# Performance work log

Measured on AMD Instinct MI355X. Metric: run time of the kernel, lower is better.

## Reference

```python
import jax, jax.numpy as jnp
import numpy as np

HIDDEN = 1024
FFN = 4096
NUM_EXPERTS = 8
LB_WEIGHT = 0.01
BATCH, SEQ = 4, 1024


def setup_inputs() -> dict:
    key = jax.random.key(0)
    ks = jax.random.split(key, 6)
    s_h = 1.0 / np.sqrt(HIDDEN)
    s_f = 1.0 / np.sqrt(FFN)
    return {
        "x": jax.random.normal(ks[0], (BATCH, SEQ, HIDDEN), dtype=jnp.float32),
        "router_w": jax.random.uniform(ks[1], (NUM_EXPERTS, HIDDEN), jnp.float32, -s_h, s_h),
        "fc1_w": jax.random.uniform(ks[2], (NUM_EXPERTS, FFN, HIDDEN), jnp.float32, -s_h, s_h),
        "fc1_b": jax.random.uniform(ks[3], (NUM_EXPERTS, FFN), jnp.float32, -s_h, s_h),
        "fc2_w": jax.random.uniform(ks[4], (NUM_EXPERTS, HIDDEN, FFN), jnp.float32, -s_f, s_f),
        "fc2_b": jax.random.uniform(ks[5], (NUM_EXPERTS, HIDDEN), jnp.float32, -s_f, s_f),
    }


def reference(x, router_w, fc1_w, fc1_b, fc2_w, fc2_b):
    B, S, H = x.shape
    E = router_w.shape[0]
    T = B * S
    xf = x.reshape(T, H)

    # Router: top-1 over softmax probs
    logits = xf @ router_w.T                     # [T, E]
    probs = jax.nn.softmax(logits, axis=-1)      # [T, E]
    expert_weights = jnp.max(probs, axis=-1)     # [T]
    expert_idx = jnp.argmax(probs, axis=-1)      # [T] int

    # Expert MLPs computed densely for all experts (faithful math; jit-friendly
    # replacement for the dynamic-shaped per-expert gather/scatter).
    h = jax.nn.gelu(jnp.einsum('td,efd->etf', xf, fc1_w) + fc1_b[:, None, :],
                    approximate=False)                      # [E, T, F]
    out_all = jnp.einsum('etf,ehf->eth', h, fc2_w) + fc2_b[:, None, :]  # [E, T, H]

    # Select each token's assigned expert output, scaled by its gate weight.
    out_flat = out_all[expert_idx, jnp.arange(T)] * expert_weights[:, None]  # [T, H]
    output = out_flat.reshape(B, S, H)

    # Load balance loss
    mean_probs = probs.mean(axis=0)                                   # [E]
    counts = jnp.bincount(expert_idx, length=E).astype(jnp.float32)   # [E]
    freq = counts / T
    aux_loss = LB_WEIGHT * E * jnp.sum(mean_probs * freq)
    return output, aux_loss
```

## Files before the change

### kernel.cpp

```cpp
#include <hip/hip_runtime.h>
#include <cstdint>

#define HID 1024
#define FFN 4096
#define NE 8
#define NT 4096

typedef __bf16 bf16x8 __attribute__((ext_vector_type(8)));
typedef unsigned short ushortx8 __attribute__((ext_vector_type(8)));
typedef float f32x4 __attribute__((ext_vector_type(4)));


__device__ __forceinline__ unsigned pk_bf16(float a, float b) {
  unsigned ua = __float_as_uint(a), ub = __float_as_uint(b);
  ua = (ua + 0x7fffu + ((ua >> 16) & 1u)) >> 16;
  ub = (ub + 0x7fffu + ((ub >> 16) & 1u)) >> 16;
  return ua | (ub << 16);
}
__device__ __forceinline__ unsigned short f2bf(float a) {
  unsigned ua = __float_as_uint(a);
  return (unsigned short)((ua + 0x7fffu + ((ua >> 16) & 1u)) >> 16);
}

__global__ __launch_bounds__(256) void router_kernel(
    const float* __restrict__ x, const float* __restrict__ rw,
    int* __restrict__ counts, float* __restrict__ prob_sum,
    int* __restrict__ eidx, float* __restrict__ wgt) {
  __shared__ float rsm[NE * HID];
  __shared__ float pshare[4][NE];
  for (int i = threadIdx.x; i < NE * HID; i += 256) rsm[i] = rw[i];
  __syncthreads();
  int wave = threadIdx.x >> 6, lane = threadIdx.x & 63;
  int t = blockIdx.x * 4 + wave;
  const float* xr = x + (size_t)t * HID;
  float acc[NE];
#pragma unroll
  for (int e = 0; e < NE; e++) acc[e] = 0.f;
#pragma unroll
  for (int j = 0; j < HID / 64; j++) {
    float xv = xr[j * 64 + lane];
#pragma unroll
    for (int e = 0; e < NE; e++) acc[e] = fmaf(xv, rsm[e * HID + j * 64 + lane], acc[e]);
  }
#pragma unroll
  for (int off = 32; off > 0; off >>= 1) {
#pragma unroll
    for (int e = 0; e < NE; e++) acc[e] += __shfl_down(acc[e], off);
  }
  if (lane == 0) {
    float mx = acc[0]; int mi = 0;
#pragma unroll
    for (int e = 1; e < NE; e++) if (acc[e] > mx) { mx = acc[e]; mi = e; }
    float pr[NE], se = 0.f;
#pragma unroll
    for (int e = 0; e < NE; e++) { pr[e] = expf(acc[e] - mx); se += pr[e]; }
    float inv = 1.f / se;
    wgt[t] = pr[mi] * inv;
    eidx[t] = mi;
    atomicAdd(&counts[mi], 1);
#pragma unroll
    for (int e = 0; e < NE; e++) pshare[wave][e] = pr[e] * inv;
  }
  __syncthreads();
  if (threadIdx.x < NE) {
    float s = pshare[0][threadIdx.x] + pshare[1][threadIdx.x] +
              pshare[2][threadIdx.x] + pshare[3][threadIdx.x];
    atomicAdd(&prob_sum[threadIdx.x], s);
  }
}

__global__ void scan_aux_kernel(const int* __restrict__ counts,
                                const float* __restrict__ prob_sum,
                                int* __restrict__ offsets,
                                float* __restrict__ aux_out) {
  if (threadIdx.x == 0) {
    int off = 0; float s = 0.f;
    for (int e = 0; e < NE; e++) {
      offsets[e] = off;
      off += counts[e];
      s += (prob_sum[e] / (float)NT) * ((float)counts[e] / (float)NT);
    }
    *aux_out = 0.01f * (float)NE * s;
  }
}

__global__ void bucketize_kernel(const int* __restrict__ eidx,
                                 const int* __restrict__ offsets,
                                 int* __restrict__ cursor, int* __restrict__ perm) {
  int t = blockIdx.x * 256 + threadIdx.x;
  int e = eidx[t];
  int slot = atomicAdd(&cursor[e], 1);
  perm[offsets[e] + slot] = t;
}

__global__ __launch_bounds__(256) void gemm1_kernel(
    const float* __restrict__ x, const float* __restrict__ w1,
    const float* __restrict__ b1, const int* __restrict__ counts,
    const int* __restrict__ offsets, const int* __restrict__ perm,
    unsigned short* __restrict__ hbuf) {
  int e = blockIdx.z;
  int Nexp = counts[e];
  int m0 = blockIdx.y * 128;
  if (m0 >= Nexp) return;
  int n0 = blockIdx.x * 128;
  int obase = offsets[e];
  int gbase = obase + m0;

  __shared__ unsigned short As[128 * 40];
  __shared__ unsigned short Bs[128 * 40];
  __shared__ int toks[128];

  int tid = threadIdx.x;
  if (tid < 128) {
    int r = m0 + tid;
    toks[tid] = perm[obase + (r < Nexp ? r : Nexp - 1)];
  }
  __syncthreads();

  int tr = tid >> 3;
  int tc = tid & 7;
  const float* w1e = w1 + (size_t)e * FFN * HID;
  const float* aptr[4];
  const float* bptr[4];
#pragma unroll
  for (int i = 0; i < 4; i++) {
    aptr[i] = x + (size_t)toks[tr + 32 * i] * HID + tc * 4;
    bptr[i] = w1e + (size_t)(n0 + tr + 32 * i) * HID + tc * 4;
  }

  int lane = tid & 63, w = tid >> 6;
  int wm = w & 1, wn = w >> 1;
  int quad = lane >> 4, l15 = lane & 15;
  f32x4 acc[4][4] = {};
  const int std_idx = tr * 40 + tc * 4;

  for (int kk = 0; kk < HID / 32; kk++) {
#pragma unroll
    for (int i = 0; i < 4; i++) {
      float4 av = *(const float4*)(aptr[i] + kk * 32);
      float4 bv = *(const float4*)(bptr[i] + kk * 32);
      uint2 ap; ap.x = pk_bf16(av.x, av.y); ap.y = pk_bf16(av.z, av.w);
      uint2 bp; bp.x = pk_bf16(bv.x, bv.y); bp.y = pk_bf16(bv.z, bv.w);
      *(uint2*)&As[std_idx + i * 32 * 40] = ap;
      *(uint2*)&Bs[std_idx + i * 32 * 40] = bp;
    }
    __syncthreads();
    bf16x8 af[4], bfr[4];
#pragma unroll
    for (int mt = 0; mt < 4; mt++) {
      ushortx8 raw = *(const ushortx8*)&As[(wm * 64 + mt * 16 + l15) * 40 + quad * 8];
      af[mt] = __builtin_bit_cast(bf16x8, raw);
    }
#pragma unroll
    for (int nt = 0; nt < 4; nt++) {
      ushortx8 raw = *(const ushortx8*)&Bs[(wn * 64 + nt * 16 + l15) * 40 + quad * 8];
      bfr[nt] = __builtin_bit_cast(bf16x8, raw);
    }
#pragma unroll
    for (int mt = 0; mt < 4; mt++)
#pragma unroll
      for (int nt = 0; nt < 4; nt++)
        acc[mt][nt] = __builtin_amdgcn_mfma_f32_16x16x32_bf16(af[mt], bfr[nt], acc[mt][nt], 0, 0, 0);
    __syncthreads();
  }

  int mrem = Nexp - m0;
#pragma unroll
  for (int mt = 0; mt < 4; mt++) {
    int rbase = wm * 64 + mt * 16 + quad * 4;
#pragma unroll
    for (int nt = 0; nt < 4; nt++) {
      int col = wn * 64 + nt * 16 + l15;
      float bb = b1[e * FFN + n0 + col];
#pragma unroll
      for (int r = 0; r < 4; r++) {
        int rr = rbase + r;
        if (rr < mrem) {
          float v = acc[mt][nt][r] + bb;
          v = 0.5f * v * (1.0f + erff(v * 0.70710678118654752f));
          hbuf[(size_t)(gbase + rr) * FFN + n0 + col] = f2bf(v);
        }
      }
    }
  }
}

__global__ __launch_bounds__(256) void gemm2_kernel(
    const unsigned short* __restrict__ hbuf, const float* __restrict__ w2,
    const float* __restrict__ b2, const int* __restrict__ counts,
    const int* __restrict__ offsets, const int* __restrict__ perm,
    const float* __restrict__ wgt, float* __restrict__ out) {
  int e = blockIdx.z;
  int Nexp = counts[e];
  int m0 = blockIdx.y * 128;
  if (m0 >= Nexp) return;
  int n0 = blockIdx.x * 128;
  int obase = offsets[e];
  int gbase = obase + m0;

  __shared__ unsigned short As[128 * 40];
  __shared__ unsigned short Bs[128 * 40];
  __shared__ int toks[128];
  __shared__ float wsh[128];

  int tid = threadIdx.x;
  if (tid < 128) {
    int r = m0 + tid;
    int tk = perm[obase + (r < Nexp ? r : Nexp - 1)];
    toks[tid] = tk;
    wsh[tid] = wgt[tk];
  }
  __syncthreads();

  int tr2 = tid >> 2, tc2 = tid & 3;
  int g0 = gbase + tr2;     if (g0 > NT - 1) g0 = NT - 1;
  int g1 = gbase + tr2 + 64; if (g1 > NT - 1) g1 = NT - 1;
  const unsigned short* ap0 = hbuf + (size_t)g0 * FFN + tc2 * 8;
  const unsigned short* ap1 = hbuf + (size_t)g1 * FFN + tc2 * 8;

  int tr = tid >> 3, tc = tid & 7;
  const float* w2e = w2 + (size_t)e * HID * FFN;
  const float* bptr[4];
#pragma unroll
  for (int i = 0; i < 4; i++)
    bptr[i] = w2e + (size_t)(n0 + tr + 32 * i) * FFN + tc * 4;

  int lane = tid & 63, w = tid >> 6;
  int wm = w & 1, wn = w >> 1;
  int quad = lane >> 4, l15 = lane & 15;
  f32x4 acc[4][4] = {};

  for (int kk = 0; kk < FFN / 32; kk++) {
    uint4 a0 = *(const uint4*)(ap0 + kk * 32);
    uint4 a1 = *(const uint4*)(ap1 + kk * 32);
    float4 bv[4];
#pragma unroll
    for (int i = 0; i < 4; i++) bv[i] = *(const float4*)(bptr[i] + kk * 32);
    *(uint4*)&As[tr2 * 40 + tc2 * 8] = a0;
    *(uint4*)&As[(tr2 + 64) * 40 + tc2 * 8] = a1;
#pragma unroll
    for (int i = 0; i < 4; i++) {
      uint2 bp; bp.x = pk_bf16(bv[i].x, bv[i].y); bp.y = pk_bf16(bv[i].z, bv[i].w);
      *(uint2*)&Bs[(tr + 32 * i) * 40 + tc * 4] = bp;
    }
    __syncthreads();
    bf16x8 af[4], bfr[4];
#pragma unroll
    for (int mt = 0; mt < 4; mt++) {
      ushortx8 raw = *(const ushortx8*)&As[(wm * 64 + mt * 16 + l15) * 40 + quad * 8];
      af[mt] = __builtin_bit_cast(bf16x8, raw);
    }
#pragma unroll
    for (int nt = 0; nt < 4; nt++) {
      ushortx8 raw = *(const ushortx8*)&Bs[(wn * 64 + nt * 16 + l15) * 40 + quad * 8];
      bfr[nt] = __builtin_bit_cast(bf16x8, raw);
    }
#pragma unroll
    for (int mt = 0; mt < 4; mt++)
#pragma unroll
      for (int nt = 0; nt < 4; nt++)
        acc[mt][nt] = __builtin_amdgcn_mfma_f32_16x16x32_bf16(af[mt], bfr[nt], acc[mt][nt], 0, 0, 0);
    __syncthreads();
  }

  int mrem = Nexp - m0;
#pragma unroll
  for (int mt = 0; mt < 4; mt++) {
    int rbase = wm * 64 + mt * 16 + quad * 4;
#pragma unroll
    for (int nt = 0; nt < 4; nt++) {
      int col = wn * 64 + nt * 16 + l15;
      float bb = b2[e * HID + n0 + col];
#pragma unroll
      for (int r = 0; r < 4; r++) {
        int rr = rbase + r;
        if (rr < mrem) {
          float v = (acc[mt][nt][r] + bb) * wsh[rr];
          out[(size_t)toks[rr] * HID + n0 + col] = v;
        }
      }
    }
  }
}

extern "C" void kernel_launch(void* const* d_in, const int* in_sizes, int n_in,
                              void* d_out, int out_size, void* d_ws, size_t ws_size,
                              hipStream_t stream) {
  const float* x  = (const float*)d_in[0];
  const float* rw = (const float*)d_in[1];
  const float* w1 = (const float*)d_in[2];
  const float* b1 = (const float*)d_in[3];
  const float* w2 = (const float*)d_in[4];
  const float* b2 = (const float*)d_in[5];
  float* out = (float*)d_out;

  char* ws = (char*)d_ws;
  int*   counts   = (int*)(ws + 0);
  int*   cursor   = (int*)(ws + 32);
  float* prob_sum = (float*)(ws + 64);
  int*   offsets  = (int*)(ws + 96);
  int*   perm     = (int*)(ws + 256);
  float* wgt      = (float*)(ws + 256 + 16384);
  int*   eidx     = (int*)(ws + 256 + 32768);
  unsigned short* hbuf = (unsigned short*)(ws + 65536);

  hipMemsetAsync(d_ws, 0, 128, stream);
  router_kernel<<<NT / 4, 256, 0, stream>>>(x, rw, counts, prob_sum, eidx, wgt);
  scan_aux_kernel<<<1, 64, 0, stream>>>(counts, prob_sum, offsets, out + (size_t)NT * HID);
  bucketize_kernel<<<NT / 256, 256, 0, stream>>>(eidx, offsets, cursor, perm);
  gemm1_kernel<<<dim3(FFN / 128, NT / 128, NE), 256, 0, stream>>>(x, w1, b1, counts, offsets, perm, hbuf);
  gemm2_kernel<<<dim3(HID / 128, NT / 128, NE), 256, 0, stream>>>(hbuf, w2, b2, counts, offsets, perm, wgt, out);
}
```

Measured before the change: 625.0 us.

## Double-buffer LDS in both expert GEMMs, narrow gemm1 tiles, split-K gemm2

Both expert GEMMs now use double-buffered shared-memory tiles, so the next k-slice's global loads are issued before the current MFMAs and written after them, hiding load latency behind one barrier per step. gemm1 narrows its N tile to 64 to launch more blocks. gemm2 splits K in two across grid z and merges the halves with float atomicAdd into an output that is zeroed beforehand. The price is an extra memset of the full output, atomic traffic on the output, more LDS per block, and non-deterministic summation order.

```diff
diff --git a/kernel.cpp b/kernel.cpp
--- a/kernel.cpp
+++ b/kernel.cpp
@@ -11,7 +11,7 @@
 typedef float f32x4 __attribute__((ext_vector_type(4)));
 
 
-__device__ __forceinline__ unsigned pk_bf16(float a, float b) {
+__device__ __forceinline__ unsigned cvt2(float a, float b) {
   unsigned ua = __float_as_uint(a), ub = __float_as_uint(b);
   ua = (ua + 0x7fffu + ((ua >> 16) & 1u)) >> 16;
   ub = (ub + 0x7fffu + ((ub >> 16) & 1u)) >> 16;
@@ -93,7 +93,7 @@
   perm[offsets[e] + slot] = t;
 }
 
-__global__ __launch_bounds__(256) void gemm1_kernel(
+__global__ __launch_bounds__(256, 4) void gemm1_kernel(
     const float* __restrict__ x, const float* __restrict__ w1,
     const float* __restrict__ b1, const int* __restrict__ counts,
     const int* __restrict__ offsets, const int* __restrict__ perm,
@@ -102,12 +102,12 @@
   int Nexp = counts[e];
   int m0 = blockIdx.y * 128;
   if (m0 >= Nexp) return;
-  int n0 = blockIdx.x * 128;
+  int n0 = blockIdx.x * 64;
   int obase = offsets[e];
   int gbase = obase + m0;
 
-  __shared__ unsigned short As[128 * 40];
-  __shared__ unsigned short Bs[128 * 40];
+  __shared__ unsigned short As[2][128 * 40];
+  __shared__ unsigned short Bs[2][64 * 40];
   __shared__ int toks[128];
 
   int tid = threadIdx.x;
@@ -117,50 +117,76 @@
   }
   __syncthreads();
 
-  int tr = tid >> 3;
-  int tc = tid & 7;
-  const float* w1e = w1 + (size_t)e * FFN * HID;
+  int tr = tid >> 3, tc = tid & 7;
+  const float* w1e = w1 + (size_t)e * (FFN * HID);
   const float* aptr[4];
-  const float* bptr[4];
-#pragma unroll
-  for (int i = 0; i < 4; i++) {
-    aptr[i] = x + (size_t)toks[tr + 32 * i] * HID + tc * 4;
-    bptr[i] = w1e + (size_t)(n0 + tr + 32 * i) * HID + tc * 4;
-  }
-
-  int lane = tid & 63, w = tid >> 6;
-  int wm = w & 1, wn = w >> 1;
+  const float* bptr[2];
+#pragma unroll
+  for (int i = 0; i < 4; i++) aptr[i] = x + (size_t)toks[tr + 32 * i] * HID + tc * 4;
+#pragma unroll
+  for (int i = 0; i < 2; i++) bptr[i] = w1e + (size_t)(n0 + tr + 32 * i) * HID + tc * 4;
+
+  int lane = tid & 63, w = tid >> 6, wm = w & 1, wn = w >> 1;
   int quad = lane >> 4, l15 = lane & 15;
-  f32x4 acc[4][4] = {};
-  const int std_idx = tr * 40 + tc * 4;
-
-  for (int kk = 0; kk < HID / 32; kk++) {
+  f32x4 acc[4][2] = {};
+  const int sidx = tr * 40 + tc * 4;
+
+  {
+    float4 pa[4], pb[2];
+#pragma unroll
+    for (int i = 0; i < 4; i++) pa[i] = *(const float4*)(aptr[i]);
+#pragma unroll
+    for (int i = 0; i < 2; i++) pb[i] = *(const float4*)(bptr[i]);
 #pragma unroll
     for (int i = 0; i < 4; i++) {
-      float4 av = *(const float4*)(aptr[i] + kk * 32);
-      float4 bv = *(const float4*)(bptr[i] + kk * 32);
-      uint2 ap; ap.x = pk_bf16(av.x, av.y); ap.y = pk_bf16(av.z, av.w);
-      uint2 bp; bp.x = pk_bf16(bv.x, bv.y); bp.y = pk_bf16(bv.z, bv.w);
-      *(uint2*)&As[std_idx + i * 32 * 40] = ap;
-      *(uint2*)&Bs[std_idx + i * 32 * 40] = bp;
-    }
-    __syncthreads();
-    bf16x8 af[4], bfr[4];
-#pragma unroll
-    for (int mt = 0; mt < 4; mt++) {
-      ushortx8 raw = *(const ushortx8*)&As[(wm * 64 + mt * 16 + l15) * 40 + quad * 8];
-      af[mt] = __builtin_bit_cast(bf16x8, raw);
-    }
-#pragma unroll
-    for (int nt = 0; nt < 4; nt++) {
-      ushortx8 raw = *(const ushortx8*)&Bs[(wn * 64 + nt * 16 + l15) * 40 + quad * 8];
-      bfr[nt] = __builtin_bit_cast(bf16x8, raw);
-    }
+      uint2 p; p.x = cvt2(pa[i].x, pa[i].y); p.y = cvt2(pa[i].z, pa[i].w);
+      *(uint2*)&As[0][sidx + i * 32 * 40] = p;
+    }
+#pragma unroll
+    for (int i = 0; i < 2; i++) {
+      uint2 p; p.x = cvt2(pb[i].x, pb[i].y); p.y = cvt2(pb[i].z, pb[i].w);
+      *(uint2*)&Bs[0][sidx + i * 32 * 40] = p;
+    }
+  }
+  __syncthreads();
+
+  const int NK = HID / 32;
+  for (int kk = 0; kk < NK; kk++) {
+    float4 na[4], nb[2];
+    bool more = (kk + 1 < NK);
+    if (more) {
+#pragma unroll
+      for (int i = 0; i < 4; i++) na[i] = *(const float4*)(aptr[i] + (kk + 1) * 32);
+#pragma unroll
+      for (int i = 0; i < 2; i++) nb[i] = *(const float4*)(bptr[i] + (kk + 1) * 32);
+    }
+    const unsigned short* Ab = As[kk & 1];
+    const unsigned short* Bb = Bs[kk & 1];
+    bf16x8 af[4], bfr[2];
 #pragma unroll
     for (int mt = 0; mt < 4; mt++)
-#pragma unroll
-      for (int nt = 0; nt < 4; nt++)
+      af[mt] = __builtin_bit_cast(bf16x8, *(const ushortx8*)&Ab[(wm * 64 + mt * 16 + l15) * 40 + quad * 8]);
+#pragma unroll
+    for (int nt = 0; nt < 2; nt++)
+      bfr[nt] = __builtin_bit_cast(bf16x8, *(const ushortx8*)&Bb[(wn * 32 + nt * 16 + l15) * 40 + quad * 8]);
+#pragma unroll
+    for (int mt = 0; mt < 4; mt++)
+#pragma unroll
+      for (int nt = 0; nt < 2; nt++)
         acc[mt][nt] = __builtin_amdgcn_mfma_f32_16x16x32_bf16(af[mt], bfr[nt], acc[mt][nt], 0, 0, 0);
+    if (more) {
+      int nbf = (kk + 1) & 1;
+#pragma unroll
+      for (int i = 0; i < 4; i++) {
+        uint2 p; p.x = cvt2(na[i].x, na[i].y); p.y = cvt2(na[i].z, na[i].w);
+        *(uint2*)&As[nbf][sidx + i * 32 * 40] = p;
+      }
+#pragma unroll
+      for (int i = 0; i < 2; i++) {
+        uint2 p; p.x = cvt2(nb[i].x, nb[i].y); p.y = cvt2(nb[i].z, nb[i].w);
+        *(uint2*)&Bs[nbf][sidx + i * 32 * 40] = p;
+      }
+    }
     __syncthreads();
   }
 
@@ -169,8 +195,8 @@
   for (int mt = 0; mt < 4; mt++) {
     int rbase = wm * 64 + mt * 16 + quad * 4;
 #pragma unroll
-    for (int nt = 0; nt < 4; nt++) {
-      int col = wn * 64 + nt * 16 + l15;
+    for (int nt = 0; nt < 2; nt++) {
+      int col = wn * 32 + nt * 16 + l15;
       float bb = b1[e * FFN + n0 + col];
 #pragma unroll
       for (int r = 0; r < 4; r++) {
@@ -185,21 +211,22 @@
   }
 }
 
-__global__ __launch_bounds__(256) void gemm2_kernel(
+__global__ __launch_bounds__(256, 3) void gemm2_kernel(
     const unsigned short* __restrict__ hbuf, const float* __restrict__ w2,
     const float* __restrict__ b2, const int* __restrict__ counts,
     const int* __restrict__ offsets, const int* __restrict__ perm,
     const float* __restrict__ wgt, float* __restrict__ out) {
-  int e = blockIdx.z;
+  int e = blockIdx.z & 7, kz = blockIdx.z >> 3;
   int Nexp = counts[e];
   int m0 = blockIdx.y * 128;
   if (m0 >= Nexp) return;
   int n0 = blockIdx.x * 128;
+  int k0 = kz * (FFN / 2);
   int obase = offsets[e];
   int gbase = obase + m0;
 
-  __shared__ unsigned short As[128 * 40];
-  __shared__ unsigned short Bs[128 * 40];
+  __shared__ unsigned short As[2][128 * 40];
+  __shared__ unsigned short Bs[2][128 * 40];
   __shared__ int toks[128];
   __shared__ float wsh[128];
 
@@ -213,53 +240,72 @@
   __syncthreads();
 
   int tr2 = tid >> 2, tc2 = tid & 3;
-  int g0 = gbase + tr2;     if (g0 > NT - 1) g0 = NT - 1;
+  int g0 = gbase + tr2;      if (g0 > NT - 1) g0 = NT - 1;
   int g1 = gbase + tr2 + 64; if (g1 > NT - 1) g1 = NT - 1;
-  const unsigned short* ap0 = hbuf + (size_t)g0 * FFN + tc2 * 8;
-  const unsigned short* ap1 = hbuf + (size_t)g1 * FFN + tc2 * 8;
+  const unsigned short* ap0 = hbuf + (size_t)g0 * FFN + k0 + tc2 * 8;
+  const unsigned short* ap1 = hbuf + (size_t)g1 * FFN + k0 + tc2 * 8;
 
   int tr = tid >> 3, tc = tid & 7;
-  const float* w2e = w2 + (size_t)e * HID * FFN;
+  const float* w2e = w2 + (size_t)e * (HID * FFN);
   const float* bptr[4];
 #pragma unroll
   for (int i = 0; i < 4; i++)
-    bptr[i] = w2e + (size_t)(n0 + tr + 32 * i) * FFN + tc * 4;
-
-  int lane = tid & 63, w = tid >> 6;
-  int wm = w & 1, wn = w >> 1;
+    bptr[i] = w2e + (size_t)(n0 + tr + 32 * i) * FFN + k0 + tc * 4;
+
+  int lane = tid & 63, w = tid >> 6, wm = w & 1, wn = w >> 1;
   int quad = lane >> 4, l15 = lane & 15;
   f32x4 acc[4][4] = {};
-
-  for (int kk = 0; kk < FFN / 32; kk++) {
-    uint4 a0 = *(const uint4*)(ap0 + kk * 32);
-    uint4 a1 = *(const uint4*)(ap1 + kk * 32);
-    float4 bv[4];
-#pragma unroll
-    for (int i = 0; i < 4; i++) bv[i] = *(const float4*)(bptr[i] + kk * 32);
-    *(uint4*)&As[tr2 * 40 + tc2 * 8] = a0;
-    *(uint4*)&As[(tr2 + 64) * 40 + tc2 * 8] = a1;
+  const int sa = tr2 * 40 + tc2 * 8;
+  const int sb = tr * 40 + tc * 4;
+
+  {
+    uint4 a0 = *(const uint4*)ap0;
+    uint4 a1 = *(const uint4*)ap1;
+    *(uint4*)&As[0][sa] = a0;
+    *(uint4*)&As[0][sa + 64 * 40] = a1;
 #pragma unroll
     for (int i = 0; i < 4; i++) {
-      uint2 bp; bp.x = pk_bf16(bv[i].x, bv[i].y); bp.y = pk_bf16(bv[i].z, bv[i].w);
-      *(uint2*)&Bs[(tr + 32 * i) * 40 + tc * 4] = bp;
-    }
-    __syncthreads();
+      float4 bv = *(const float4*)bptr[i];
+      uint2 p; p.x = cvt2(bv.x, bv.y); p.y = cvt2(bv.z, bv.w);
+      *(uint2*)&Bs[0][sb + i * 32 * 40] = p;
+    }
+  }
+  __syncthreads();
+
+  const int NK = (FFN / 2) / 32;
+  for (int kk = 0; kk < NK; kk++) {
+    uint4 na0, na1; float4 nb[4];
+    bool more = (kk + 1 < NK);
+    if (more) {
+      na0 = *(const uint4*)(ap0 + (kk + 1) * 32);
+      na1 = *(const uint4*)(ap1 + (kk + 1) * 32);
+#pragma unroll
+      for (int i = 0; i < 4; i++) nb[i] = *(const float4*)(bptr[i] + (kk + 1) * 32);
+    }
+    const unsigned short* Ab = As[kk & 1];
+    const unsigned short* Bb = Bs[kk & 1];
     bf16x8 af[4], bfr[4];
 #pragma unroll
-    for (int mt = 0; mt < 4; mt++) {
-      ushortx8 raw = *(const ushortx8*)&As[(wm * 64 + mt * 16 + l15) * 40 + quad * 8];
-      af[mt] = __builtin_bit_cast(bf16x8, raw);
-    }
-#pragma unroll
-    for (int nt = 0; nt < 4; nt++) {
-      ushortx8 raw = *(const ushortx8*)&Bs[(wn * 64 + nt * 16 + l15) * 40 + quad * 8];
-      bfr[nt] = __builtin_bit_cast(bf16x8, raw);
-    }
+    for (int mt = 0; mt < 4; mt++)
+      af[mt] = __builtin_bit_cast(bf16x8, *(const ushortx8*)&Ab[(wm * 64 + mt * 16 + l15) * 40 + quad * 8]);
+#pragma unroll
+    for (int nt = 0; nt < 4; nt++)
+      bfr[nt] = __builtin_bit_cast(bf16x8, *(const ushortx8*)&Bb[(wn * 64 + nt * 16 + l15) * 40 + quad * 8]);
 #pragma unroll
     for (int mt = 0; mt < 4; mt++)
 #pragma unroll
       for (int nt = 0; nt < 4; nt++)
         acc[mt][nt] = __builtin_amdgcn_mfma_f32_16x16x32_bf16(af[mt], bfr[nt], acc[mt][nt], 0, 0, 0);
+    if (more) {
+      int nbf = (kk + 1) & 1;
+      *(uint4*)&As[nbf][sa] = na0;
+      *(uint4*)&As[nbf][sa + 64 * 40] = na1;
+#pragma unroll
+      for (int i = 0; i < 4; i++) {
+        uint2 p; p.x = cvt2(nb[i].x, nb[i].y); p.y = cvt2(nb[i].z, nb[i].w);
+        *(uint2*)&Bs[nbf][sb + i * 32 * 40] = p;
+      }
+    }
     __syncthreads();
   }
 
@@ -275,8 +321,9 @@
       for (int r = 0; r < 4; r++) {
         int rr = rbase + r;
         if (rr < mrem) {
-          float v = (acc[mt][nt][r] + bb) * wsh[rr];
-          out[(size_t)toks[rr] * HID + n0 + col] = v;
+          float v = acc[mt][nt][r];
+          if (kz == 0) v += bb;
+          atomicAdd(out + (size_t)toks[rr] * HID + n0 + col, v * wsh[rr]);
         }
       }
     }
@@ -304,10 +351,11 @@
   int*   eidx     = (int*)(ws + 256 + 32768);
   unsigned short* hbuf = (unsigned short*)(ws + 65536);
 
-  hipMemsetAsync(d_ws, 0, 128, stream);
+  (void)hipMemsetAsync(d_ws, 0, 128, stream);
+  (void)hipMemsetAsync(d_out, 0, (size_t)(NT * HID + 1) * sizeof(float), stream);
   router_kernel<<<NT / 4, 256, 0, stream>>>(x, rw, counts, prob_sum, eidx, wgt);
   scan_aux_kernel<<<1, 64, 0, stream>>>(counts, prob_sum, offsets, out + (size_t)NT * HID);
   bucketize_kernel<<<NT / 256, 256, 0, stream>>>(eidx, offsets, cursor, perm);
-  gemm1_kernel<<<dim3(FFN / 128, NT / 128, NE), 256, 0, stream>>>(x, w1, b1, counts, offsets, perm, hbuf);
-  gemm2_kernel<<<dim3(HID / 128, NT / 128, NE), 256, 0, stream>>>(hbuf, w2, b2, counts, offsets, perm, wgt, out);
-}
+  gemm1_kernel<<<dim3(FFN / 64, NT / 128, NE), 256, 0, stream>>>(x, w1, b1, counts, offsets, perm, hbuf);
+  gemm2_kernel<<<dim3(HID / 128, NT / 128, NE * 2), 256, 0, stream>>>(hbuf, w2, b2, counts, offsets, perm, wgt, out);
+}
```

After: 553.3 us. 1.13x faster.
